# Kernel optimization log

Measured on AMD Instinct MI355X. Metric: run time of the kernel, lower is better.

## Reference

```python
import jax, jax.numpy as jnp
import numpy as np

N_EMBD = 1024
N_HEAD = 16
EPS = 1e-5


def _layernorm(x, g, b):
    mu = jnp.mean(x, axis=-1, keepdims=True)
    var = jnp.mean(jnp.square(x - mu), axis=-1, keepdims=True)
    return (x - mu) * jax.lax.rsqrt(var + EPS) * g + b


def setup_inputs() -> dict:
    key = jax.random.key(0)
    ks = jax.random.split(key, 8)
    e = N_EMBD
    s = 0.02
    return {
        "x": jax.random.normal(ks[0], (4, 2048, e), dtype=jnp.float32),
        "ln1_g": jnp.ones((e,), jnp.float32),
        "ln1_b": jnp.zeros((e,), jnp.float32),
        "w_attn": jax.random.normal(ks[1], (e, 3 * e), jnp.float32) * s,
        "b_attn": jnp.zeros((3 * e,), jnp.float32),
        "w_proj": jax.random.normal(ks[2], (e, e), jnp.float32) * s,
        "b_proj": jnp.zeros((e,), jnp.float32),
        "ln2_g": jnp.ones((e,), jnp.float32),
        "ln2_b": jnp.zeros((e,), jnp.float32),
        "w_fc": jax.random.normal(ks[3], (e, 4 * e), jnp.float32) * s,
        "b_fc": jnp.zeros((4 * e,), jnp.float32),
        "w_fc2": jax.random.normal(ks[4], (4 * e, e), jnp.float32) * s,
        "b_fc2": jnp.zeros((e,), jnp.float32),
    }


def reference(x, ln1_g, ln1_b, w_attn, b_attn, w_proj, b_proj,
              ln2_g, ln2_b, w_fc, b_fc, w_fc2, b_fc2):
    b, s, e = x.shape
    h = N_HEAD
    d = e // h

    # --- attention sublayer (pre-LN) ---
    xn = _layernorm(x, ln1_g, ln1_b)
    qkv = xn @ w_attn + b_attn                      # [b, s, 3e]
    qkv = qkv.reshape(b, s, 3, h, d)
    q = jnp.transpose(qkv[:, :, 0], (0, 2, 1, 3))   # [b, h, s, d]
    k = jnp.transpose(qkv[:, :, 1], (0, 2, 1, 3))
    v = jnp.transpose(qkv[:, :, 2], (0, 2, 1, 3))

    mask = jnp.triu(jnp.ones((s, s), x.dtype), k=1) * jnp.asarray(-1e10, x.dtype)
    attn = jnp.einsum('bhqd,bhkd->bhqk', q, k) / jnp.sqrt(jnp.asarray(d, x.dtype))
    attn = jax.nn.softmax(attn + mask, axis=-1)
    out = jnp.einsum('bhqk,bhkd->bhqd', attn, v)    # [b, h, s, d]
    out = jnp.transpose(out, (0, 2, 1, 3)).reshape(b, s, e)
    x = x + (out @ w_proj + b_proj)

    # --- MLP sublayer (pre-LN) ---
    xn = _layernorm(x, ln2_g, ln2_b)
    hdn = jax.nn.gelu(xn @ w_fc + b_fc, approximate=False)
    x = x + (hdn @ w_fc2 + b_fc2)
    return x
```

## Files before the change

### kernel.cpp

```cpp
#include <hip/hip_runtime.h>

typedef unsigned short u16;
typedef unsigned int u32;
typedef __attribute__((ext_vector_type(8))) short bf16x8;
typedef __attribute__((ext_vector_type(4))) float f32x4;
typedef __attribute__((ext_vector_type(4))) u32 u32x4;

#define DEV __device__ __forceinline__
#define MFMA16(a, b, c) __builtin_amdgcn_mfma_f32_16x16x32_bf16(a, b, c, 0, 0, 0)

DEV u16 f2bf(float f) {
  u32 u = __float_as_uint(f);
  u32 r = (u + 0x7fffu + ((u >> 16) & 1u)) >> 16;
  return (u16)r;
}

DEV void async16(const void* g, void* l) {
  __builtin_amdgcn_global_load_lds((const __attribute__((address_space(1))) u32*)g,
                                   (__attribute__((address_space(3))) u32*)l, 16, 0, 0);
}

__global__ __launch_bounds__(256)
void wt_transpose(const float* __restrict__ w, u16* __restrict__ wt, int K, int N) {
  __shared__ float tile[32][33];
  int n0 = blockIdx.x * 32;
  int k0 = blockIdx.y * 32;
  int tx = threadIdx.x;
  int ty = threadIdx.y;
#pragma unroll
  for (int i = 0; i < 4; ++i)
    tile[ty + 8 * i][tx] = w[(size_t)(k0 + ty + 8 * i) * N + n0 + tx];
  __syncthreads();
#pragma unroll
  for (int i = 0; i < 4; ++i) {
    int n = ty + 8 * i;
    wt[(size_t)(n0 + n) * K + k0 + tx] = f2bf(tile[tx][n]);
  }
}

__global__ __launch_bounds__(256)
void ln_kernel(const float* __restrict__ x, const float* __restrict__ g,
               const float* __restrict__ b, u16* __restrict__ out) {
  int row = blockIdx.x;
  int tid = threadIdx.x;
  const float4* xr = (const float4*)(x + (size_t)row * 1024);
  float4 v = xr[tid];
  float s = v.x + v.y + v.z + v.w;
  float ss = v.x * v.x + v.y * v.y + v.z * v.z + v.w * v.w;
#pragma unroll
  for (int o = 32; o > 0; o >>= 1) {
    s += __shfl_down(s, o);
    ss += __shfl_down(ss, o);
  }
  __shared__ float ps[4], pss[4];
  if ((tid & 63) == 0) { ps[tid >> 6] = s; pss[tid >> 6] = ss; }
  __syncthreads();
  s = ps[0] + ps[1] + ps[2] + ps[3];
  ss = pss[0] + pss[1] + pss[2] + pss[3];
  float mu = s * (1.0f / 1024.0f);
  float var = ss * (1.0f / 1024.0f) - mu * mu;
  float rs = rsqrtf(var + 1e-5f);
  float4 gg = ((const float4*)g)[tid];
  float4 bb = ((const float4*)b)[tid];
  ushort4 ov;
  ov.x = f2bf((v.x - mu) * rs * gg.x + bb.x);
  ov.y = f2bf((v.y - mu) * rs * gg.y + bb.y);
  ov.z = f2bf((v.z - mu) * rs * gg.z + bb.z);
  ov.w = f2bf((v.w - mu) * rs * gg.w + bb.w);
  *(ushort4*)(out + (size_t)row * 1024 + tid * 4) = ov;
}

__global__ __launch_bounds__(256)
void v_transpose(const u16* __restrict__ v, u16* __restrict__ vt) {
  __shared__ u16 t[64][72];
  int s0 = blockIdx.x * 64;
  int bh = blockIdx.y;
  int tid = threadIdx.x;
  const u16* src = v + ((size_t)bh * 2048 + s0) * 64;
#pragma unroll
  for (int p = 0; p < 2; ++p) {
    int r = p * 32 + (tid >> 3);
    int c = (tid & 7) * 8;
    u32x4 a = *(const u32x4*)(src + r * 64 + c);
    const u16* pa = (const u16*)&a;
#pragma unroll
    for (int j = 0; j < 8; ++j) t[r][c + j] = pa[j];
  }
  __syncthreads();
  u16* dst = vt + (size_t)bh * 131072 + s0;
#pragma unroll
  for (int p = 0; p < 2; ++p) {
    int d = p * 32 + (tid >> 3);
    int sc = (tid & 7) * 8;
    u32x4 a;
    u16* pa = (u16*)&a;
#pragma unroll
    for (int j = 0; j < 8; ++j) pa[j] = t[sc + j][d];
    *(u32x4*)(dst + (size_t)d * 2048 + sc) = a;
  }
}

template <int EPI>
__global__ __launch_bounds__(256, 2)
void gemm128(const u16* __restrict__ A, const u16* __restrict__ Bt,
             const float* __restrict__ bias, int M, int N, int K,
             float* __restrict__ outf, u16* __restrict__ outb,
             const float* __restrict__ res,
             u16* __restrict__ qp, u16* __restrict__ kp, u16* __restrict__ vp) {
  __shared__ char lds[32768];
  const int tid = threadIdx.x;
  const int lane = tid & 63, wid = tid >> 6;
  const int wr = wid >> 1, wc = wid & 1;
  const int lr = lane & 15, hi = lane >> 4;
  const int swz = (lr & 7) << 4;

  const int nbx = gridDim.x;
  int lin = blockIdx.x + nbx * blockIdx.y;
  int xcd = lin & 7, j = lin >> 3;
  int bx = j % nbx;
  int by = xcd * 8 + j / nbx;

  const long m0 = (long)by * 128;
  const long n0 = (long)bx * 128;
  const long ldb = (long)K * 2;
  const char* Abase = (const char*)A + m0 * ldb;
  const char* Bbase = (const char*)Bt + n0 * ldb;

  f32x4 acc[4][4];
#pragma unroll
  for (int i = 0; i < 4; ++i)
#pragma unroll
    for (int jj = 0; jj < 4; ++jj) acc[i][jj] = (f32x4)0.0f;

  auto stage = [&](const char* base, int kt, int dst) {
#pragma unroll
    for (int l = 0; l < 4; ++l) {
      int c = (wid * 4 + l) * 64 + lane;
      int r = c >> 3, ch = c & 7;
      async16(base + (long)kt * 128 + (long)r * ldb + ((ch * 16) ^ ((r & 7) << 4)),
              lds + dst + (wid * 4 + l) * 1024);
    }
  };
  auto rdA = [&](int mi, int kk) {
    int rr = wr * 64 + mi * 16 + lr;
    return *(const bf16x8*)(lds + rr * 128 + ((kk * 64 + hi * 16) ^ swz));
  };
  auto rdB = [&](int ni, int kk) {
    int rr = wc * 64 + ni * 16 + lr;
    return *(const bf16x8*)(lds + 16384 + rr * 128 + ((kk * 64 + hi * 16) ^ swz));
  };

  const int NT = K >> 6;
  for (int kt = 0; kt < NT; ++kt) {
    stage(Abase, kt, 0);
    stage(Bbase, kt, 16384);
    __syncthreads();
    bf16x8 a[4][2], b[4][2];
#pragma unroll
    for (int mi = 0; mi < 4; ++mi) { a[mi][0] = rdA(mi, 0); a[mi][1] = rdA(mi, 1); }
#pragma unroll
    for (int ni = 0; ni < 4; ++ni) { b[ni][0] = rdB(ni, 0); b[ni][1] = rdB(ni, 1); }
    __builtin_amdgcn_s_setprio(1);
#pragma unroll
    for (int kk = 0; kk < 2; ++kk)
#pragma unroll
      for (int mi = 0; mi < 4; ++mi)
#pragma unroll
        for (int ni = 0; ni < 4; ++ni)
          acc[mi][ni] = MFMA16(a[mi][kk], b[ni][kk], acc[mi][ni]);
    __builtin_amdgcn_s_setprio(0);
    __syncthreads();
  }

  int rgrp = hi * 4;
#pragma unroll
  for (int mi = 0; mi < 4; ++mi) {
#pragma unroll
    for (int ni = 0; ni < 4; ++ni) {
      long col = n0 + wc * 64 + ni * 16 + lr;
      float bv = bias[col];
#pragma unroll
      for (int r = 0; r < 4; ++r) {
        long row = m0 + wr * 64 + mi * 16 + rgrp + r;
        float c = acc[mi][ni][r] + bv;
        if (EPI == 0) {
          int part = (int)(col >> 10);
          int hd = (int)(col & 1023);
          long bq = row >> 11;
          long sq = row & 2047;
          long dst = (((bq << 4) + (hd >> 6)) * 2048 + sq) * 64 + (hd & 63);
          if (part == 0) qp[dst] = f2bf(c * 0.125f);
          else if (part == 1) kp[dst] = f2bf(c);
          else vp[dst] = f2bf(c);
        } else if (EPI == 1) {
          long idx = row * (long)N + col;
          outf[idx] = c + res[idx];
        } else {
          float gl = 0.5f * c * (1.0f + erff(c * 0.70710678118f));
          outb[row * (long)N + col] = f2bf(gl);
        }
      }
    }
  }
}

__global__ __launch_bounds__(256, 2)
void attn_kernel(const u16* __restrict__ q, const u16* __restrict__ k,
                 const u16* __restrict__ vt, u16* __restrict__ outp) {
  __shared__ char ldsK[2][8192];
  __shared__ char ldsV[2][8192];
  __shared__ char ldsP[4][4096];
  int lin = blockIdx.x + 8 * blockIdx.y;
  int xcd = lin & 7, pos = lin >> 3;
  int j = pos >> 3;
  int bh = ((pos & 7) << 3) | xcd;
  int tid = threadIdx.x, lane = tid & 63, w = tid >> 6;
  const u16* qb = q + (size_t)bh * 131072;
  const u16* kb = k + (size_t)bh * 131072;
  const u16* vb = vt + (size_t)bh * 131072;

  int lr = lane & 15, lg = lane >> 4;
  int swz = (lr & 7) << 4;

  const int qih = 15 - j, qil = j;
  const int NTH = 2 * qih + 2;
  const int NTL = 2 * qil + 2;

  const bf16x8 ones = (bf16x8)(short)0x3F80;

  bf16x8 qf[2][2][2];
#pragma unroll
  for (int p = 0; p < 2; ++p) {
    int q0p = (p ? qil : qih) * 128;
#pragma unroll
    for (int fq = 0; fq < 2; ++fq) {
      const u16* qr = qb + (size_t)(q0p + w * 32 + fq * 16 + lr) * 64 + lg * 8;
      qf[p][fq][0] = *(const bf16x8*)(qr);
      qf[p][fq][1] = *(const bf16x8*)(qr + 32);
    }
  }

  f32x4 o[2][2][4];
  f32x4 lacc[2][2];
  float m_run[2][2][4];
#pragma unroll
  for (int p = 0; p < 2; ++p)
#pragma unroll
    for (int fq = 0; fq < 2; ++fq) {
      lacc[p][fq] = (f32x4)0.0f;
#pragma unroll
      for (int i = 0; i < 4; ++i) {
        o[p][fq][i] = (f32x4)0.0f;
        m_run[p][fq][i] = -1e30f;
      }
    }

  auto stage = [&](int buf, int t) {
    int kv0 = t * 64;
    const char* gk = (const char*)(kb + (size_t)kv0 * 64);
#pragma unroll
    for (int i = 0; i < 2; ++i) {
      int off = i * 4096 + tid * 16;
      int src = off ^ (((off >> 7) & 7) << 4);
      async16(gk + src, &ldsK[buf][i * 4096 + w * 1024]);
    }
#pragma unroll
    for (int i = 0; i < 2; ++i) {
      int vrow = i * 32 + (tid >> 3);
      int cb = ((tid & 7) * 16) ^ ((vrow & 7) << 4);
      async16((const char*)vb + (size_t)vrow * 4096 + (size_t)kv0 * 2 + cb,
              &ldsV[buf][i * 4096 + w * 1024]);
    }
  };

  stage(0, 0);
  __syncthreads();
  int cur = 0;

  for (int t = 0; t < NTH; ++t) {
    if (t + 1 < NTH) stage(cur ^ 1, t + 1);
    int kv0 = t * 64;

#pragma unroll
    for (int p = 0; p < 2; ++p) {
      if (p == 1 && t >= NTL) break;
      int q0p = (p ? qil : qih) * 128;
      int ntp = p ? NTL : NTH;

      f32x4 s[2][4];
      __builtin_amdgcn_s_setprio(1);
#pragma unroll
      for (int nf = 0; nf < 4; ++nf) {
#pragma unroll
        for (int fq = 0; fq < 2; ++fq) s[fq][nf] = (f32x4)0.0f;
#pragma unroll
        for (int ks = 0; ks < 2; ++ks) {
          bf16x8 kf = *(const bf16x8*)(&ldsK[cur][(nf * 16 + lr) * 128 +
                                                 ((ks * 64 + lg * 16) ^ swz)]);
#pragma unroll
          for (int fq = 0; fq < 2; ++fq)
            s[fq][nf] = MFMA16(qf[p][fq][ks], kf, s[fq][nf]);
        }
      }
      __builtin_amdgcn_s_setprio(0);

      if (t + 2 >= ntp) {
#pragma unroll
        for (int fq = 0; fq < 2; ++fq)
#pragma unroll
          for (int nf = 0; nf < 4; ++nf)
#pragma unroll
            for (int r = 0; r < 4; ++r) {
              int qrow = q0p + w * 32 + fq * 16 + lg * 4 + r;
              int kvc = kv0 + nf * 16 + lr;
              if (kvc > qrow) s[fq][nf][r] = -1e30f;
            }
      }

      float pmx[2][4];
      bool need = false;
#pragma unroll
      for (int fq = 0; fq < 2; ++fq)
#pragma unroll
        for (int r = 0; r < 4; ++r) {
          pmx[fq][r] = fmaxf(fmaxf(s[fq][0][r], s[fq][1][r]),
                             fmaxf(s[fq][2][r], s[fq][3][r]));
          need = need || (pmx[fq][r] > m_run[p][fq][r] + 8.0f);
        }
      if (__any(need)) {
#pragma unroll
        for (int fq = 0; fq < 2; ++fq)
#pragma unroll
          for (int r = 0; r < 4; ++r) {
            float pm = pmx[fq][r];
#pragma unroll
            for (int m = 1; m < 16; m <<= 1) pm = fmaxf(pm, __shfl_xor(pm, m));
            float mnew = fmaxf(m_run[p][fq][r], pm);
            float al = __expf(m_run[p][fq][r] - mnew);
            m_run[p][fq][r] = mnew;
            lacc[p][fq][r] *= al;
#pragma unroll
            for (int nf = 0; nf < 4; ++nf) o[p][fq][nf][r] *= al;
          }
      }

#pragma unroll
      for (int fq = 0; fq < 2; ++fq)
#pragma unroll
        for (int nf = 0; nf < 4; ++nf)
#pragma unroll
          for (int r = 0; r < 4; ++r) {
            float pv = __expf(s[fq][nf][r] - m_run[p][fq][r]);
            int prow = fq * 16 + lg * 4 + r;
            int pb = ((nf * 16 + lr) * 2) ^ ((prow & 7) << 4);
            *(u16*)(&ldsP[w][prow * 128 + pb]) = (u16)(__float_as_uint(pv) >> 16);
          }

      __builtin_amdgcn_s_setprio(1);
#pragma unroll
      for (int ks = 0; ks < 2; ++ks) {
        bf16x8 pf[2];
#pragma unroll
        for (int fq = 0; fq < 2; ++fq)
          pf[fq] = *(const bf16x8*)(&ldsP[w][(fq * 16 + lr) * 128 +
                                             ((ks * 64 + lg * 16) ^ swz)]);
        lacc[p][0] = MFMA16(pf[0], ones, lacc[p][0]);
        lacc[p][1] = MFMA16(pf[1], ones, lacc[p][1]);
#pragma unroll
        for (int nf = 0; nf < 4; ++nf) {
          bf16x8 vf = *(const bf16x8*)(&ldsV[cur][(nf * 16 + lr) * 128 +
                                                 ((ks * 64 + lg * 16) ^ swz)]);
#pragma unroll
          for (int fq = 0; fq < 2; ++fq)
            o[p][fq][nf] = MFMA16(pf[fq], vf, o[p][fq][nf]);
        }
      }
      __builtin_amdgcn_s_setprio(0);
    }

    __syncthreads();
    cur ^= 1;
  }

  int b = bh >> 4, h = bh & 15;
#pragma unroll
  for (int p = 0; p < 2; ++p) {
    int q0p = (p ? qil : qih) * 128;
#pragma unroll
    for (int fq = 0; fq < 2; ++fq)
#pragma unroll
      for (int r = 0; r < 4; ++r) {
        int qrow = q0p + w * 32 + fq * 16 + lg * 4 + r;
        float inv = 1.0f / lacc[p][fq][r];
        size_t base = ((size_t)(b * 2048 + qrow)) * 1024 + h * 64;
#pragma unroll
        for (int nf = 0; nf < 4; ++nf)
          outp[base + nf * 16 + lr] = f2bf(o[p][fq][nf][r] * inv);
      }
  }
}

extern "C" void kernel_launch(void* const* d_in, const int* in_sizes, int n_in,
                              void* d_out, int out_size, void* d_ws, size_t ws_size,
                              hipStream_t stream) {
  const float* x      = (const float*)d_in[0];
  const float* ln1_g  = (const float*)d_in[1];
  const float* ln1_b  = (const float*)d_in[2];
  const float* w_attn = (const float*)d_in[3];
  const float* b_attn = (const float*)d_in[4];
  const float* w_proj = (const float*)d_in[5];
  const float* b_proj = (const float*)d_in[6];
  const float* ln2_g  = (const float*)d_in[7];
  const float* ln2_b  = (const float*)d_in[8];
  const float* w_fc   = (const float*)d_in[9];
  const float* b_fc   = (const float*)d_in[10];
  const float* w_fc2  = (const float*)d_in[11];
  const float* b_fc2  = (const float*)d_in[12];
  float* out = (float*)d_out;

  char* ws = (char*)d_ws;
  u16* wt_attn = (u16*)(ws + 0);
  u16* wt_proj = (u16*)(ws + 6291456);
  u16* wt_fc   = (u16*)(ws + 8388608);
  u16* wt_fc2  = (u16*)(ws + 16777216);
  u16* xn      = (u16*)(ws + 25165824);
  float* x2    = (float*)(ws + 41943040);
  char* region = ws + 75497472;
  u16* qb = (u16*)(region);
  u16* kb = (u16*)(region + 16777216);
  u16* vb = (u16*)(region + 33554432);
  u16* vt = (u16*)(region + 50331648);
  u16* ao = (u16*)(region + 67108864);
  u16* hm = (u16*)(region);

  dim3 tb(32, 8);
  wt_transpose<<<dim3(3072 / 32, 1024 / 32), tb, 0, stream>>>(w_attn, wt_attn, 1024, 3072);
  wt_transpose<<<dim3(1024 / 32, 1024 / 32), tb, 0, stream>>>(w_proj, wt_proj, 1024, 1024);
  wt_transpose<<<dim3(4096 / 32, 1024 / 32), tb, 0, stream>>>(w_fc, wt_fc, 1024, 4096);
  wt_transpose<<<dim3(1024 / 32, 4096 / 32), tb, 0, stream>>>(w_fc2, wt_fc2, 4096, 1024);

  ln_kernel<<<8192, 256, 0, stream>>>(x, ln1_g, ln1_b, xn);

  gemm128<0><<<dim3(3072 / 128, 8192 / 128), 256, 0, stream>>>(
      xn, wt_attn, b_attn, 8192, 3072, 1024,
      nullptr, nullptr, nullptr, qb, kb, vb);

  v_transpose<<<dim3(32, 64), 256, 0, stream>>>(vb, vt);

  attn_kernel<<<dim3(8, 64), 256, 0, stream>>>(qb, kb, vt, ao);

  gemm128<1><<<dim3(1024 / 128, 8192 / 128), 256, 0, stream>>>(
      ao, wt_proj, b_proj, 8192, 1024, 1024,
      x2, nullptr, x, nullptr, nullptr, nullptr);

  ln_kernel<<<8192, 256, 0, stream>>>(x2, ln2_g, ln2_b, xn);

  gemm128<2><<<dim3(4096 / 128, 8192 / 128), 256, 0, stream>>>(
      xn, wt_fc, b_fc, 8192, 4096, 1024,
      nullptr, hm, nullptr, nullptr, nullptr, nullptr);

  gemm128<1><<<dim3(1024 / 128, 8192 / 128), 256, 0, stream>>>(
      hm, wt_fc2, b_fc2, 8192, 1024, 4096,
      out, nullptr, x2, nullptr, nullptr, nullptr);
}
```

Before: 371.3 us.

## Add 128x64 GEMM for N=1024 projections and raise GEMM occupancy

Adds a gemm_n64 kernel with 128x64 tiles and uses it for the attention output projection and the second MLP GEMM, where N=1024. This doubles the block count from 512 to 1024 so the CUs are better filled. It also raises launch bounds to 4 waves per SIMD and splits the per-k fragment loads in gemm128 to cut register pressure. The smaller tiles lower data reuse per block and add more global traffic, and the tighter register budget could cause spills.

```diff
diff --git a/kernel.cpp b/kernel.cpp
--- a/kernel.cpp
+++ b/kernel.cpp
@@ -101,7 +101,7 @@
 }
 
 template <int EPI>
-__global__ __launch_bounds__(256, 2)
+__global__ __launch_bounds__(256, 4)
 void gemm128(const u16* __restrict__ A, const u16* __restrict__ Bt,
              const float* __restrict__ bias, int M, int N, int K,
              float* __restrict__ outf, u16* __restrict__ outb,
@@ -155,20 +155,21 @@
     stage(Abase, kt, 0);
     stage(Bbase, kt, 16384);
     __syncthreads();
-    bf16x8 a[4][2], b[4][2];
-#pragma unroll
-    for (int mi = 0; mi < 4; ++mi) { a[mi][0] = rdA(mi, 0); a[mi][1] = rdA(mi, 1); }
-#pragma unroll
-    for (int ni = 0; ni < 4; ++ni) { b[ni][0] = rdB(ni, 0); b[ni][1] = rdB(ni, 1); }
-    __builtin_amdgcn_s_setprio(1);
-#pragma unroll
-    for (int kk = 0; kk < 2; ++kk)
+#pragma unroll
+    for (int kk = 0; kk < 2; ++kk) {
+      bf16x8 a[4], b[4];
+#pragma unroll
+      for (int mi = 0; mi < 4; ++mi) a[mi] = rdA(mi, kk);
+#pragma unroll
+      for (int ni = 0; ni < 4; ++ni) b[ni] = rdB(ni, kk);
+      __builtin_amdgcn_s_setprio(1);
 #pragma unroll
       for (int mi = 0; mi < 4; ++mi)
 #pragma unroll
         for (int ni = 0; ni < 4; ++ni)
-          acc[mi][ni] = MFMA16(a[mi][kk], b[ni][kk], acc[mi][ni]);
-    __builtin_amdgcn_s_setprio(0);
+          acc[mi][ni] = MFMA16(a[mi], b[ni], acc[mi][ni]);
+      __builtin_amdgcn_s_setprio(0);
+    }
     __syncthreads();
   }
 
@@ -204,6 +205,98 @@
   }
 }
 
+__global__ __launch_bounds__(256, 4)
+void gemm_n64(const u16* __restrict__ A, const u16* __restrict__ Bt,
+              const float* __restrict__ bias, int M, int N, int K,
+              float* __restrict__ outf, const float* __restrict__ res) {
+  __shared__ char lds[24576];
+  const int tid = threadIdx.x;
+  const int lane = tid & 63, wid = tid >> 6;
+  const int wr = wid >> 1, wc = wid & 1;
+  const int lr = lane & 15, hi = lane >> 4;
+  const int swz = (lr & 7) << 4;
+
+  const int nbx = gridDim.x;
+  int lin = blockIdx.x + nbx * blockIdx.y;
+  int xcd = lin & 7, j = lin >> 3;
+  int bx = j % nbx;
+  int by = xcd * 8 + j / nbx;
+
+  const long m0 = (long)by * 128;
+  const long n0 = (long)bx * 64;
+  const long ldb = (long)K * 2;
+  const char* Abase = (const char*)A + m0 * ldb;
+  const char* Bbase = (const char*)Bt + n0 * ldb;
+
+  f32x4 acc[4][2];
+#pragma unroll
+  for (int i = 0; i < 4; ++i) { acc[i][0] = (f32x4)0.0f; acc[i][1] = (f32x4)0.0f; }
+
+  auto stageA = [&](int kt) {
+#pragma unroll
+    for (int l = 0; l < 4; ++l) {
+      int c = (wid * 4 + l) * 64 + lane;
+      int r = c >> 3, ch = c & 7;
+      async16(Abase + (long)kt * 128 + (long)r * ldb + ((ch * 16) ^ ((r & 7) << 4)),
+              lds + (wid * 4 + l) * 1024);
+    }
+  };
+  auto stageB = [&](int kt) {
+#pragma unroll
+    for (int l = 0; l < 2; ++l) {
+      int c = (wid * 2 + l) * 64 + lane;
+      int r = c >> 3, ch = c & 7;
+      async16(Bbase + (long)kt * 128 + (long)r * ldb + ((ch * 16) ^ ((r & 7) << 4)),
+              lds + 16384 + (wid * 2 + l) * 1024);
+    }
+  };
+  auto rdA = [&](int mi, int kk) {
+    int rr = wr * 64 + mi * 16 + lr;
+    return *(const bf16x8*)(lds + rr * 128 + ((kk * 64 + hi * 16) ^ swz));
+  };
+  auto rdB = [&](int ni, int kk) {
+    int rr = wc * 32 + ni * 16 + lr;
+    return *(const bf16x8*)(lds + 16384 + rr * 128 + ((kk * 64 + hi * 16) ^ swz));
+  };
+
+  const int NT = K >> 6;
+  for (int kt = 0; kt < NT; ++kt) {
+    stageA(kt);
+    stageB(kt);
+    __syncthreads();
+#pragma unroll
+    for (int kk = 0; kk < 2; ++kk) {
+      bf16x8 a[4], b[2];
+#pragma unroll
+      for (int mi = 0; mi < 4; ++mi) a[mi] = rdA(mi, kk);
+      b[0] = rdB(0, kk); b[1] = rdB(1, kk);
+      __builtin_amdgcn_s_setprio(1);
+#pragma unroll
+      for (int mi = 0; mi < 4; ++mi) {
+        acc[mi][0] = MFMA16(a[mi], b[0], acc[mi][0]);
+        acc[mi][1] = MFMA16(a[mi], b[1], acc[mi][1]);
+      }
+      __builtin_amdgcn_s_setprio(0);
+    }
+    __syncthreads();
+  }
+
+#pragma unroll
+  for (int mi = 0; mi < 4; ++mi) {
+#pragma unroll
+    for (int ni = 0; ni < 2; ++ni) {
+      long col = n0 + wc * 32 + ni * 16 + lr;
+      float bv = bias[col];
+#pragma unroll
+      for (int r = 0; r < 4; ++r) {
+        long row = m0 + wr * 64 + mi * 16 + hi * 4 + r;
+        long idx = row * (long)N + col;
+        outf[idx] = acc[mi][ni][r] + bv + res[idx];
+      }
+    }
+  }
+}
+
 __global__ __launch_bounds__(256, 2)
 void attn_kernel(const u16* __restrict__ q, const u16* __restrict__ k,
                  const u16* __restrict__ vt, u16* __restrict__ outp) {
@@ -449,9 +542,8 @@
 
   attn_kernel<<<dim3(8, 64), 256, 0, stream>>>(qb, kb, vt, ao);
 
-  gemm128<1><<<dim3(1024 / 128, 8192 / 128), 256, 0, stream>>>(
-      ao, wt_proj, b_proj, 8192, 1024, 1024,
-      x2, nullptr, x, nullptr, nullptr, nullptr);
+  gemm_n64<<<dim3(1024 / 64, 8192 / 128), 256, 0, stream>>>(
+      ao, wt_proj, b_proj, 8192, 1024, 1024, x2, x);
 
   ln_kernel<<<8192, 256, 0, stream>>>(x2, ln2_g, ln2_b, xn);
 
@@ -459,7 +551,6 @@
       xn, wt_fc, b_fc, 8192, 4096, 1024,
       nullptr, hm, nullptr, nullptr, nullptr, nullptr);
 
-  gemm128<1><<<dim3(1024 / 128, 8192 / 128), 256, 0, stream>>>(
-      hm, wt_fc2, b_fc2, 8192, 1024, 4096,
-      out, nullptr, x2, nullptr, nullptr, nullptr);
-}
+  gemm_n64<<<dim3(1024 / 64, 8192 / 128), 256, 0, stream>>>(
+      hm, wt_fc2, b_fc2, 8192, 1024, 4096, out, x2);
+}
```

Result: slower. 379.7 us (+2.3%).
